# Kernel tuning notes

Measured on AMD Instinct MI355X. Metric: run time of the kernel, lower is better.

The kernel has to match this reference:

```python
import jax, jax.numpy as jnp
import numpy as np

N, E, G = 50000, 800000, 64
IN, H, ED, OUT = 32, 96, 16, 128
EPS_GEN = 1e-7   # GENConv message eps
EPS_BN = 1e-5    # BatchNorm1d eps


def _bn(x, g, b):
    # training-mode BatchNorm1d: batch stats, biased variance
    mu = jnp.mean(x, axis=0)
    var = jnp.var(x, axis=0)
    return (x - mu) * jax.lax.rsqrt(var + EPS_BN) * g + b


def _genconv(x_src, x_dst, src, dst, ea, mw1, mg, mb, mw2):
    # message: relu(x_j + e_ij) + eps            [E, H]
    msg = jax.nn.relu(x_src[src] + ea) + EPS_GEN
    n = x_dst.shape[0]
    # softmax aggregation over incoming edges per dst node (t=1.0)
    m = jax.ops.segment_max(msg, dst, num_segments=n)
    ex = jnp.exp(msg - m[dst])
    s = jax.ops.segment_sum(ex, dst, num_segments=n)
    agg = jax.ops.segment_sum(msg * (ex / s[dst]), dst, num_segments=n)
    h = agg + x_dst
    # GENConv internal MLP: Lin(H,2H,no bias) -> BN -> ReLU -> Lin(2H,H,no bias)
    h = jax.nn.relu(_bn(h @ mw1, mg, mb))
    return h @ mw2


def _forward(x, edge_attr, w_src1, w_dst1, w_edge1,
             mlp1_w1, mlp1_g, mlp1_b, mlp1_w2, bn1_g, bn1_b,
             w_edge2, mlp2_w1, mlp2_g, mlp2_b, mlp2_w2, bn2_g, bn2_b,
             w_edge3, mlp3_w1, mlp3_g, mlp3_b, mlp3_w2, bn3_g, bn3_b,
             lin_w, lin_b, edge_index, batch):
    src, dst = edge_index[0], edge_index[1]
    h = _genconv(x @ w_src1, x @ w_dst1, src, dst, edge_attr @ w_edge1,
                 mlp1_w1, mlp1_g, mlp1_b, mlp1_w2)
    h = jax.nn.relu(_bn(h, bn1_g, bn1_b))
    h = _genconv(h, h, src, dst, edge_attr @ w_edge2,
                 mlp2_w1, mlp2_g, mlp2_b, mlp2_w2)
    h = jax.nn.relu(_bn(h, bn2_g, bn2_b))
    h = _genconv(h, h, src, dst, edge_attr @ w_edge3,
                 mlp3_w1, mlp3_g, mlp3_b, mlp3_w2)
    h = jax.nn.relu(_bn(h, bn3_g, bn3_b))
    # global mean pool over graphs (dropout is identity in eval)
    cnt = jax.ops.segment_sum(jnp.ones((h.shape[0],), h.dtype), batch, num_segments=G)
    pooled = jax.ops.segment_sum(h, batch, num_segments=G) / jnp.maximum(cnt, 1.0)[:, None]
    return pooled @ lin_w + lin_b


def setup_inputs() -> dict:
    key = jax.random.key(0)
    ks = jax.random.split(key, 20)
    rn = lambda i, shp, s=0.05: jax.random.normal(ks[i], shp, jnp.float32) * s
    return {
        'x': rn(0, (N, IN), 1.0),
        'edge_attr': rn(1, (E, ED), 1.0),
        'edge_index': jax.random.randint(ks[2], (2, E), 0, N, jnp.int32),
        'batch': jnp.sort(jax.random.randint(ks[3], (N,), 0, G, jnp.int32)),
        'w_src1': rn(4, (IN, H)), 'w_dst1': rn(5, (IN, H)), 'w_edge1': rn(6, (ED, H)),
        'mlp1_w1': rn(7, (H, 2 * H)), 'mlp1_g': jnp.ones(2 * H), 'mlp1_b': jnp.zeros(2 * H),
        'mlp1_w2': rn(8, (2 * H, H)), 'bn1_g': jnp.ones(H), 'bn1_b': jnp.zeros(H),
        'w_edge2': rn(9, (ED, H)),
        'mlp2_w1': rn(10, (H, 2 * H)), 'mlp2_g': jnp.ones(2 * H), 'mlp2_b': jnp.zeros(2 * H),
        'mlp2_w2': rn(11, (2 * H, H)), 'bn2_g': jnp.ones(H), 'bn2_b': jnp.zeros(H),
        'w_edge3': rn(12, (ED, H)),
        'mlp3_w1': rn(13, (H, 2 * H)), 'mlp3_g': jnp.ones(2 * H), 'mlp3_b': jnp.zeros(2 * H),
        'mlp3_w2': rn(14, (2 * H, H)), 'bn3_g': jnp.ones(H), 'bn3_b': jnp.zeros(H),
        'lin_w': rn(15, (H, OUT)), 'lin_b': jnp.zeros(OUT),
    }


def reference(x, edge_attr, edge_index, batch, w_src1, w_dst1, w_edge1,
              mlp1_w1, mlp1_g, mlp1_b, mlp1_w2, bn1_g, bn1_b,
              w_edge2, mlp2_w1, mlp2_g, mlp2_b, mlp2_w2, bn2_g, bn2_b,
              w_edge3, mlp3_w1, mlp3_g, mlp3_b, mlp3_w2, bn3_g, bn3_b,
              lin_w, lin_b):
    return _forward(x, edge_attr, w_src1, w_dst1, w_edge1,
                    mlp1_w1, mlp1_g, mlp1_b, mlp1_w2, bn1_g, bn1_b,
                    w_edge2, mlp2_w1, mlp2_g, mlp2_b, mlp2_w2, bn2_g, bn2_b,
                    w_edge3, mlp3_w1, mlp3_g, mlp3_b, mlp3_w2, bn3_g, bn3_b,
                    lin_w, lin_b, edge_index, batch)
```

## Files before the change

### kernel.cpp

```cpp
#include <hip/hip_runtime.h>
#include <math.h>

#define NN 50000
#define EE 800000
#define GG 64
#define HH 96
#define H2 192
#define INF 32
#define EDF 16
#define OUTF 128
#define EPS_GEN 1e-7f
#define EPS_BN 1e-5f
#define NPB 100
#define NB_SCAN 49
#define NBH (256 * NB_SCAN)
#define LOG2E 1.44269504088896f
#define SHIFT2 28.85390081777927f

typedef _Float16 f16;
typedef _Float16 f16x2 __attribute__((ext_vector_type(2)));
typedef _Float16 f16x8 __attribute__((ext_vector_type(8)));
typedef float f32x4 __attribute__((ext_vector_type(4)));

static inline size_t align256(size_t x) { return (x + 255) & ~(size_t)255; }

__device__ __forceinline__ float fdot2(f16x2 a, f16x2 b, float c) {
#if __has_builtin(__builtin_amdgcn_fdot2)
    return __builtin_amdgcn_fdot2(a, b, c, false);
#else
    return fmaf((float)a.x, (float)b.x, fmaf((float)a.y, (float)b.y, c));
#endif
}

__device__ __forceinline__ float exp2fast(float x) {
#if __has_builtin(__builtin_amdgcn_exp2f)
    return __builtin_amdgcn_exp2f(x);
#else
    return exp2f(x);
#endif
}


__global__ __launch_bounds__(256) void hist_kernel(const int* __restrict__ dst,
                                                   int* __restrict__ deg) {
    int e = blockIdx.x * 256 + threadIdx.x;
    if (e >= EE) return;
    atomicAdd(&deg[dst[e]], 1);
}

__global__ __launch_bounds__(1024) void scan1_kernel(const int* __restrict__ deg,
                                                     int* __restrict__ offs,
                                                     int* __restrict__ bsum,
                                                     int* __restrict__ bhist) {
    __shared__ int ws[16];
    __shared__ int lh[256];
    int tid = threadIdx.x, lane = tid & 63, w = tid >> 6;
    if (tid < 256) lh[tid] = 0;
    int i = blockIdx.x * 1024 + tid;
    int v = (i < NN) ? deg[i] : 0;
    __syncthreads();
    if (i < NN) {
        int b = 255 - (v > 255 ? 255 : v);
        atomicAdd(&lh[b], 1);
    }
    int x = v;
    #pragma unroll
    for (int off = 1; off < 64; off <<= 1) {
        int y = __shfl_up(x, off, 64);
        if (lane >= off) x += y;
    }
    if (lane == 63) ws[w] = x;
    __syncthreads();
    int wpre = 0;
    for (int j = 0; j < w; ++j) wpre += ws[j];
    if (i < NN) offs[i] = wpre + x - v;
    if (tid == 1023) bsum[blockIdx.x] = wpre + x;
    if (tid < 256) bhist[tid * NB_SCAN + blockIdx.x] = lh[tid];
}

__global__ __launch_bounds__(64) void scan2_kernel(int* __restrict__ bsum) {
    int lane = threadIdx.x;
    int v = (lane < NB_SCAN) ? bsum[lane] : 0;
    int x = v;
    #pragma unroll
    for (int off = 1; off < 64; off <<= 1) {
        int y = __shfl_up(x, off, 64);
        if (lane >= off) x += y;
    }
    if (lane < NB_SCAN) bsum[lane] = x - v;
}

__global__ __launch_bounds__(256) void scan3_kernel(int* __restrict__ offs,
                                                    const int* __restrict__ bsum) {
    int i = blockIdx.x * 256 + threadIdx.x;
    if (i < NN) offs[i] += bsum[i >> 10];
    if (i == 0) offs[NN] = EE;
}

__global__ __launch_bounds__(1024) void bscan_kernel(int* __restrict__ bhist) {
    __shared__ int ws[16];
    __shared__ int carry_s;
    int tid = threadIdx.x, lane = tid & 63, w = tid >> 6;
    if (tid == 0) carry_s = 0;
    __syncthreads();
    for (int base = 0; base < NBH; base += 1024) {
        int i = base + tid;
        int v = (i < NBH) ? bhist[i] : 0;
        int x = v;
        #pragma unroll
        for (int off = 1; off < 64; off <<= 1) {
            int y = __shfl_up(x, off, 64);
            if (lane >= off) x += y;
        }
        if (lane == 63) ws[w] = x;
        __syncthreads();
        int wpre = 0;
        for (int j = 0; j < w; ++j) wpre += ws[j];
        int carry = carry_s;
        if (i < NBH) bhist[i] = carry + wpre + x - v;
        __syncthreads();
        if (tid == 1023) carry_s = carry + wpre + x;
        __syncthreads();
    }
}

__global__ __launch_bounds__(1024) void dscatter_kernel(const int* __restrict__ deg,
                                                        const int* __restrict__ bhist,
                                                        int* __restrict__ perm) {
    __shared__ int cnt[256];
    int tid = threadIdx.x;
    if (tid < 256) cnt[tid] = 0;
    __syncthreads();
    int n = blockIdx.x * 1024 + tid;
    if (n < NN) {
        int d = deg[n];
        int b = 255 - (d > 255 ? 255 : d);
        int rank = atomicAdd(&cnt[b], 1);
        perm[bhist[b * NB_SCAN + blockIdx.x] + rank] = n;
    }
}

__global__ __launch_bounds__(256) void scatter_kernel(const int* __restrict__ src,
                                                      const int* __restrict__ dst,
                                                      const int* __restrict__ offs,
                                                      int* __restrict__ cnt2,
                                                      const float* __restrict__ eattr,
                                                      int* __restrict__ csr_src,
                                                      float4* __restrict__ csrea) {
    int e = blockIdx.x * 256 + threadIdx.x;
    if (e >= EE) return;
    int d = dst[e];
    int slot = offs[d] + atomicAdd(&cnt2[d], 1);
    csr_src[slot] = src[e];
    const float4* ep = (const float4*)(eattr + (size_t)e * EDF);
    float4 v0 = ep[0], v1 = ep[1], v2 = ep[2], v3 = ep[3];
    union { f16x2 h[4]; float4 f; } a, b;
    a.h[0] = f16x2{(f16)v0.x, (f16)v0.y};
    a.h[1] = f16x2{(f16)v0.z, (f16)v0.w};
    a.h[2] = f16x2{(f16)v1.x, (f16)v1.y};
    a.h[3] = f16x2{(f16)v1.z, (f16)v1.w};
    b.h[0] = f16x2{(f16)v2.x, (f16)v2.y};
    b.h[1] = f16x2{(f16)v2.z, (f16)v2.w};
    b.h[2] = f16x2{(f16)v3.x, (f16)v3.y};
    b.h[3] = f16x2{(f16)v3.z, (f16)v3.w};
    csrea[(size_t)slot * 2] = a.f;
    csrea[(size_t)slot * 2 + 1] = b.f;
}

__global__ __launch_bounds__(256) void wprep_kernel(
    const float* __restrict__ we0, const float* __restrict__ we1, const float* __restrict__ we2,
    const float* __restrict__ m10, const float* __restrict__ m11, const float* __restrict__ m12,
    const float* __restrict__ m20, const float* __restrict__ m21, const float* __restrict__ m22,
    f16* __restrict__ wte, f16* __restrict__ wt1, f16* __restrict__ wt2) {
    int idx = blockIdx.x * 256 + threadIdx.x;
    if (idx < 4608) {
        const float* w = (idx < 1536) ? we0 : ((idx < 3072) ? we1 : we2);
        int r = idx % 1536, c = r / EDF, k = r % EDF;
        wte[idx] = (f16)w[k * HH + c];
    } else if (idx < 4608 + 3 * 18432) {
        int m = idx - 4608;
        const float* w = (m < 18432) ? m10 : ((m < 36864) ? m11 : m12);
        int r = m % 18432, j = r / HH, k = r % HH;
        wt1[m] = (f16)w[k * H2 + j];
    } else if (idx < 4608 + 6 * 18432) {
        int m = idx - 4608 - 3 * 18432;
        const float* w = (m < 18432) ? m20 : ((m < 36864) ? m21 : m22);
        int r = m % 18432, j = r / H2, k = r % H2;
        wt2[m] = (f16)w[k * HH + j];
    }
}


__global__ __launch_bounds__(256) void proj_kernel(const float* __restrict__ x,
                                                   const float* __restrict__ ws,
                                                   const float* __restrict__ wd,
                                                   f16* __restrict__ xs,
                                                   f16* __restrict__ xd) {
    __shared__ float Ws[INF * HH], Wd[INF * HH];
    int tid = threadIdx.x;
    for (int i = tid; i < INF * HH; i += 256) { Ws[i] = ws[i]; Wd[i] = wd[i]; }
    __syncthreads();
    int gid = blockIdx.x * 256 + tid;
    if (gid >= NN * HH) return;
    int n = gid / HH, c = gid % HH;
    const float* xr = x + (size_t)n * INF;
    float as = 0.f, ad = 0.f;
    #pragma unroll
    for (int k = 0; k < INF; ++k) {
        float xv = xr[k];
        as = fmaf(xv, Ws[k * HH + c], as);
        ad = fmaf(xv, Wd[k * HH + c], ad);
    }
    xs[gid] = (f16)as;
    xd[gid] = (f16)ad;
}


__global__ __launch_bounds__(192) void agg_kernel(const f16* __restrict__ xsrc,
                                                  const f16* __restrict__ xdst,
                                                  const float4* __restrict__ csrea,
                                                  const f16* __restrict__ wt,
                                                  const int* __restrict__ offs,
                                                  const int* __restrict__ csr_src,
                                                  const int* __restrict__ perm,
                                                  f16* __restrict__ hpre) {
    int tid = threadIdx.x;
    int idx = blockIdx.x * 8 + tid / 24;
    if (idx >= NN) return;
    int node = perm[idx];
    int cg = tid % 24, c0 = cg * 4;
    union W8 { float4 f[2]; f16x2 h[8]; };
    W8 w[4];
    #pragma unroll
    for (int cc = 0; cc < 4; ++cc) {
        const float4* wp = (const float4*)(wt + (c0 + cc) * EDF);
        w[cc].f[0] = wp[0];
        w[cc].f[1] = wp[1];
    }
    int s0 = offs[node], s1 = offs[node + 1];
    float num[4] = {0.f, 0.f, 0.f, 0.f}, den[4] = {0.f, 0.f, 0.f, 0.f};
    if (s0 < s1) {
        int last = s1 - 1;
        union EA { float4 f; f16x2 h[4]; };
        union XU { float2 f; f16x2 h[2]; };
        int j1 = (s0 + 1 < last) ? s0 + 1 : last;
        int j2 = (s0 + 2 < last) ? s0 + 2 : last;
        int sA = csr_src[s0];
        int sB = csr_src[j1];
        int sC = csr_src[j2];
        EA eA0, eA1, eB0, eB1;
        eA0.f = csrea[(size_t)s0 * 2];
        eA1.f = csrea[(size_t)s0 * 2 + 1];
        eB0.f = csrea[(size_t)j1 * 2];
        eB1.f = csrea[(size_t)j1 * 2 + 1];
        XU xA, xB;
        xA.f = *(const float2*)(xsrc + (size_t)sA * HH + c0);
        xB.f = *(const float2*)(xsrc + (size_t)sB * HH + c0);
        for (int j = s0; j <= last; ++j) {
            int j2n = (j + 2 < last) ? j + 2 : last;
            int j3n = (j + 3 < last) ? j + 3 : last;
            EA eC0, eC1;
            XU xC;
            eC0.f = csrea[(size_t)j2n * 2];
            eC1.f = csrea[(size_t)j2n * 2 + 1];
            xC.f = *(const float2*)(xsrc + (size_t)sC * HH + c0);
            int sD = csr_src[j3n];
            float xv[4] = {(float)xA.h[0].x, (float)xA.h[0].y,
                           (float)xA.h[1].x, (float)xA.h[1].y};
            #pragma unroll
            for (int cc = 0; cc < 4; ++cc) {
                float acc = 0.f;
                #pragma unroll
                for (int k = 0; k < 4; ++k) acc = fdot2(eA0.h[k], w[cc].h[k], acc);
                #pragma unroll
                for (int k = 0; k < 4; ++k) acc = fdot2(eA1.h[k], w[cc].h[4 + k], acc);
                float msg = fmaxf(xv[cc] + acc, 0.f) + EPS_GEN;
                float p = exp2fast(fmaf(msg, LOG2E, -SHIFT2));
                den[cc] += p;
                num[cc] = fmaf(msg, p, num[cc]);
            }
            eA0 = eB0; eA1 = eB1; eB0 = eC0; eB1 = eC1;
            xA = xB; xB = xC;
            sC = sD;
        }
    }
    union { float2 f; f16x2 h[2]; } xd, o;
    xd.f = *(const float2*)(xdst + (size_t)node * HH + c0);
    float xdv[4] = {(float)xd.h[0].x, (float)xd.h[0].y, (float)xd.h[1].x, (float)xd.h[1].y};
    float r0 = (den[0] > 0.f) ? num[0] / den[0] : 0.f;
    float r1 = (den[1] > 0.f) ? num[1] / den[1] : 0.f;
    float r2 = (den[2] > 0.f) ? num[2] / den[2] : 0.f;
    float r3 = (den[3] > 0.f) ? num[3] / den[3] : 0.f;
    o.h[0] = f16x2{(f16)(r0 + xdv[0]), (f16)(r1 + xdv[1])};
    o.h[1] = f16x2{(f16)(r2 + xdv[2]), (f16)(r3 + xdv[3])};
    *(float2*)(hpre + (size_t)node * HH + c0) = o.f;
}

#define LDA1 104

__global__ __launch_bounds__(256) void gemm1_kernel(const f16* __restrict__ A,
                                                    const f16* __restrict__ Wt,
                                                    f16* __restrict__ T,
                                                    float* __restrict__ colsum,
                                                    float* __restrict__ colsumsq) {
    __shared__ f16 Al[64 * LDA1];
    __shared__ f16 Wl[192 * LDA1];
    __shared__ float red[H2 * 2];
    int tid = threadIdx.x, n0 = blockIdx.x * 64;
    for (int v = tid; v < 64 * 12; v += 256) {
        int r = v / 12, c8 = (v % 12) * 8;
        float4 d = {0.f, 0.f, 0.f, 0.f};
        if (n0 + r < NN) d = *(const float4*)(A + (size_t)(n0 + r) * HH + c8);
        *(float4*)(Al + r * LDA1 + c8) = d;
    }
    for (int v = tid; v < 192 * 12; v += 256) {
        int r = v / 12, c8 = (v % 12) * 8;
        *(float4*)(Wl + r * LDA1 + c8) = *(const float4*)(Wt + r * HH + c8);
    }
    if (tid < H2) { red[tid] = 0.f; red[H2 + tid] = 0.f; }
    __syncthreads();
    int wv = tid >> 6, l = tid & 63, lr = l & 15, lg = l >> 4;
    int i0 = wv * 16;
    f32x4 acc[12];
    #pragma unroll
    for (int t = 0; t < 12; ++t) acc[t] = (f32x4){0.f, 0.f, 0.f, 0.f};
    #pragma unroll
    for (int ks = 0; ks < 3; ++ks) {
        int k0 = ks * 32 + lg * 8;
        f16x8 af = *(const f16x8*)(Al + (i0 + lr) * LDA1 + k0);
        #pragma unroll
        for (int t = 0; t < 12; ++t) {
            f16x8 bf = *(const f16x8*)(Wl + (t * 16 + lr) * LDA1 + k0);
            acc[t] = __builtin_amdgcn_mfma_f32_16x16x32_f16(af, bf, acc[t], 0, 0, 0);
        }
    }
    #pragma unroll
    for (int t = 0; t < 12; ++t) {
        int col = t * 16 + lr;
        float s = 0.f, q = 0.f;
        #pragma unroll
        for (int rr = 0; rr < 4; ++rr) {
            int row = n0 + i0 + lg * 4 + rr;
            float v = acc[t][rr];
            if (row < NN) {
                T[(size_t)row * H2 + col] = (f16)v;
                s += v;
                q = fmaf(v, v, q);
            }
        }
        s += __shfl_xor(s, 16); s += __shfl_xor(s, 32);
        q += __shfl_xor(q, 16); q += __shfl_xor(q, 32);
        if (lg == 0) { atomicAdd(&red[col], s); atomicAdd(&red[H2 + col], q); }
    }
    __syncthreads();
    if (tid < H2) {
        atomicAdd(&colsum[tid], red[tid]);
        atomicAdd(&colsumsq[tid], red[H2 + tid]);
    }
}

#define LDA2 200

__global__ __launch_bounds__(256) void gemm2_kernel(const f16* __restrict__ T,
                                                    const f16* __restrict__ Wt,
                                                    const float* __restrict__ cs1,
                                                    const float* __restrict__ cq1,
                                                    const float* __restrict__ g1,
                                                    const float* __restrict__ b1,
                                                    f16* __restrict__ U,
                                                    float* __restrict__ colsum,
                                                    float* __restrict__ colsumsq) {
    __shared__ f16 Al[64 * LDA2];
    __shared__ f16 Wl[96 * LDA2];
    __shared__ float ab[H2 * 2];
    __shared__ float red[HH * 2];
    int tid = threadIdx.x, n0 = blockIdx.x * 64;
    if (tid < H2) {
        const float invN = 1.f / (float)NN;
        float mu = cs1[tid] * invN;
        float var = fmaxf(cq1[tid] * invN - mu * mu, 0.f);
        float a = g1[tid] * rsqrtf(var + EPS_BN);
        ab[tid] = a;
        ab[H2 + tid] = b1[tid] - mu * a;
    }
    if (tid < HH) { red[tid] = 0.f; red[HH + tid] = 0.f; }
    __syncthreads();
    for (int v = tid; v < 64 * 24; v += 256) {
        int r = v / 24, c8 = (v % 24) * 8;
        float4 dd = {0.f, 0.f, 0.f, 0.f};
        if (n0 + r < NN) {
            union { float4 f; f16x2 h[4]; } u, o;
            u.f = *(const float4*)(T + (size_t)(n0 + r) * H2 + c8);
            #pragma unroll
            for (int p = 0; p < 4; ++p) {
                float x0 = fmaxf(fmaf((float)u.h[p].x, ab[c8 + 2 * p], ab[H2 + c8 + 2 * p]), 0.f);
                float x1 = fmaxf(fmaf((float)u.h[p].y, ab[c8 + 2 * p + 1], ab[H2 + c8 + 2 * p + 1]), 0.f);
                o.h[p] = f16x2{(f16)x0, (f16)x1};
            }
            dd = o.f;
        }
        *(float4*)(Al + r * LDA2 + c8) = dd;
    }
    for (int v = tid; v < 96 * 24; v += 256) {
        int r = v / 24, c8 = (v % 24) * 8;
        *(float4*)(Wl + r * LDA2 + c8) = *(const float4*)(Wt + r * H2 + c8);
    }
    __syncthreads();
    int wv = tid >> 6, l = tid & 63, lr = l & 15, lg = l >> 4;
    int i0 = wv * 16;
    f32x4 acc[6];
    #pragma unroll
    for (int t = 0; t < 6; ++t) acc[t] = (f32x4){0.f, 0.f, 0.f, 0.f};
    #pragma unroll
    for (int ks = 0; ks < 6; ++ks) {
        int k0 = ks * 32 + lg * 8;
        f16x8 af = *(const f16x8*)(Al + (i0 + lr) * LDA2 + k0);
        #pragma unroll
        for (int t = 0; t < 6; ++t) {
            f16x8 bf = *(const f16x8*)(Wl + (t * 16 + lr) * LDA2 + k0);
            acc[t] = __builtin_amdgcn_mfma_f32_16x16x32_f16(af, bf, acc[t], 0, 0, 0);
        }
    }
    #pragma unroll
    for (int t = 0; t < 6; ++t) {
        int col = t * 16 + lr;
        float s = 0.f, q = 0.f;
        #pragma unroll
        for (int rr = 0; rr < 4; ++rr) {
            int row = n0 + i0 + lg * 4 + rr;
            float v = acc[t][rr];
            if (row < NN) {
                U[(size_t)row * HH + col] = (f16)v;
                s += v;
                q = fmaf(v, v, q);
            }
        }
        s += __shfl_xor(s, 16); s += __shfl_xor(s, 32);
        q += __shfl_xor(q, 16); q += __shfl_xor(q, 32);
        if (lg == 0) { atomicAdd(&red[col], s); atomicAdd(&red[HH + col], q); }
    }
    __syncthreads();
    if (tid < HH) {
        atomicAdd(&colsum[tid], red[tid]);
        atomicAdd(&colsumsq[tid], red[HH + tid]);
    }
}


__global__ __launch_bounds__(256) void elem_kernel(const f16* __restrict__ U,
                                                   const float* __restrict__ cs2,
                                                   const float* __restrict__ cq2,
                                                   const float* __restrict__ g2,
                                                   const float* __restrict__ b2,
                                                   f16* __restrict__ Hout) {
    __shared__ float ab[HH * 2];
    int tid = threadIdx.x;
    if (tid < HH) {
        const float invN = 1.f / (float)NN;
        float mu = cs2[tid] * invN;
        float var = fmaxf(cq2[tid] * invN - mu * mu, 0.f);
        float a = g2[tid] * rsqrtf(var + EPS_BN);
        ab[tid] = a;
        ab[HH + tid] = b2[tid] - mu * a;
    }
    __syncthreads();
    int i = blockIdx.x * 256 + tid;
    if (i >= NN * HH / 8) return;
    union { float4 f; f16x2 h[4]; } u, o;
    u.f = ((const float4*)U)[i];
    int k = (i % 12) * 8;
    #pragma unroll
    for (int p = 0; p < 4; ++p) {
        float x0 = fmaxf(fmaf((float)u.h[p].x, ab[k + 2 * p], ab[HH + k + 2 * p]), 0.f);
        float x1 = fmaxf(fmaf((float)u.h[p].y, ab[k + 2 * p + 1], ab[HH + k + 2 * p + 1]), 0.f);
        o.h[p] = f16x2{(f16)x0, (f16)x1};
    }
    ((float4*)Hout)[i] = o.f;
}


__global__ __launch_bounds__(192) void pool_bn_kernel(const f16* __restrict__ U,
                                                      const float* __restrict__ cs2,
                                                      const float* __restrict__ cq2,
                                                      const float* __restrict__ g2,
                                                      const float* __restrict__ b2,
                                                      const int* __restrict__ batch,
                                                      float* __restrict__ pool) {
    __shared__ float ab[HH * 2];
    int tid = threadIdx.x;
    if (tid < HH) {
        const float invN = 1.f / (float)NN;
        float mu = cs2[tid] * invN;
        float var = fmaxf(cq2[tid] * invN - mu * mu, 0.f);
        float a = g2[tid] * rsqrtf(var + EPS_BN);
        ab[tid] = a;
        ab[HH + tid] = b2[tid] - mu * a;
    }
    __syncthreads();
    int n0 = blockIdx.x * NPB;
    int n1 = (n0 + NPB < NN) ? n0 + NPB : NN;
    int c = tid % HH;
    int h = tid / HH;
    float a_ = ab[c], b_ = ab[HH + c];
    float acc = 0.f;
    int gcur = -1;
    for (int n = n0 + h; n < n1; n += 2) {
        int g = batch[n];
        if (g != gcur) {
            if (gcur >= 0) atomicAdd(&pool[gcur * HH + c], acc);
            acc = 0.f;
            gcur = g;
        }
        acc += fmaxf(fmaf((float)U[(size_t)n * HH + c], a_, b_), 0.f);
    }
    if (gcur >= 0) atomicAdd(&pool[gcur * HH + c], acc);
}

__global__ __launch_bounds__(128) void out_kernel(const float* __restrict__ pool,
                                                  const int* __restrict__ batch,
                                                  const float* __restrict__ lw,
                                                  const float* __restrict__ lb,
                                                  float* __restrict__ out) {
    int g = blockIdx.x, o = threadIdx.x;
    int lo = 0, hi = NN;
    while (lo < hi) { int mid = (lo + hi) >> 1; if (batch[mid] < g) lo = mid + 1; else hi = mid; }
    int s = lo;
    lo = 0; hi = NN;
    while (lo < hi) { int mid = (lo + hi) >> 1; if (batch[mid] < g + 1) lo = mid + 1; else hi = mid; }
    float inv = 1.f / fmaxf((float)(lo - s), 1.f);
    float acc = lb[o];
    for (int c = 0; c < HH; ++c) acc = fmaf(pool[g * HH + c] * inv, lw[c * OUTF + o], acc);
    out[(size_t)g * OUTF + o] = acc;
}


extern "C" void kernel_launch(void* const* d_in, const int* in_sizes, int n_in,
                              void* d_out, int out_size, void* d_ws, size_t ws_size,
                              hipStream_t stream) {
    const float* x = (const float*)d_in[0];
    const float* eattr = (const float*)d_in[1];
    const int* eidx = (const int*)d_in[2];
    const int* batch = (const int*)d_in[3];
    const float* w_src1 = (const float*)d_in[4];
    const float* w_dst1 = (const float*)d_in[5];
    const float* w_e[3] = {(const float*)d_in[6], (const float*)d_in[13], (const float*)d_in[20]};
    const float* mw1[3] = {(const float*)d_in[7], (const float*)d_in[14], (const float*)d_in[21]};
    const float* mg[3] = {(const float*)d_in[8], (const float*)d_in[15], (const float*)d_in[22]};
    const float* mb[3] = {(const float*)d_in[9], (const float*)d_in[16], (const float*)d_in[23]};
    const float* mw2[3] = {(const float*)d_in[10], (const float*)d_in[17], (const float*)d_in[24]};
    const float* bng[3] = {(const float*)d_in[11], (const float*)d_in[18], (const float*)d_in[25]};
    const float* bnb[3] = {(const float*)d_in[12], (const float*)d_in[19], (const float*)d_in[26]};
    const float* lin_w = (const float*)d_in[27];
    const float* lin_b = (const float*)d_in[28];
    float* out = (float*)d_out;

    const int* src = eidx;
    const int* dst = eidx + EE;

    char* base = (char*)d_ws;
    size_t off = 0;
    int* deg = (int*)(base + off); off = align256(off + (size_t)NN * 4);
    int* cnt2 = (int*)(base + off); off = align256(off + (size_t)NN * 4);
    int* offs = (int*)(base + off); off = align256(off + (size_t)(NN + 1) * 4);
    int* bsum = (int*)(base + off); off = align256(off + (size_t)NB_SCAN * 4);
    int* bhist = (int*)(base + off); off = align256(off + (size_t)NBH * 4);
    int* perm = (int*)(base + off); off = align256(off + (size_t)NN * 4);
    int* csr_src = (int*)(base + off); off = align256(off + (size_t)EE * 4);
    float* stats = (float*)(base + off); off = align256(off + 576 * 4);
    float* colsum1 = stats;
    float* colsumsq1 = stats + 192;
    float* colsum2 = stats + 384;
    float* colsumsq2 = stats + 480;
    float* pool = (float*)(base + off); off = align256(off + (size_t)GG * HH * 4);
    f16* wte = (f16*)(base + off); off = align256(off + (size_t)3 * 1536 * 2);
    f16* wt1 = (f16*)(base + off); off = align256(off + (size_t)3 * 18432 * 2);
    f16* wt2 = (f16*)(base + off); off = align256(off + (size_t)3 * 18432 * 2);
    f16* XS = (f16*)(base + off); off = align256(off + (size_t)NN * HH * 2);
    f16* XD = (f16*)(base + off); off = align256(off + (size_t)NN * HH * 2);
    f16* HP = (f16*)(base + off); off = align256(off + (size_t)NN * HH * 2);
    f16* T = (f16*)(base + off); off = align256(off + (size_t)NN * H2 * 2);
    float4* csrea = (float4*)(base + off); off = align256(off + (size_t)EE * 32);
    (void)in_sizes; (void)n_in; (void)out_size; (void)ws_size;

    hipMemsetAsync(deg, 0, (size_t)NN * 4, stream);
    hipMemsetAsync(cnt2, 0, (size_t)NN * 4, stream);
    hist_kernel<<<(EE + 255) / 256, 256, 0, stream>>>(dst, deg);
    scan1_kernel<<<NB_SCAN, 1024, 0, stream>>>(deg, offs, bsum, bhist);
    scan2_kernel<<<1, 64, 0, stream>>>(bsum);
    scan3_kernel<<<(NN + 255) / 256, 256, 0, stream>>>(offs, bsum);
    bscan_kernel<<<1, 1024, 0, stream>>>(bhist);
    dscatter_kernel<<<NB_SCAN, 1024, 0, stream>>>(deg, bhist, perm);
    scatter_kernel<<<(EE + 255) / 256, 256, 0, stream>>>(src, dst, offs, cnt2, eattr,
                                                         csr_src, csrea);
    wprep_kernel<<<(4608 + 6 * 18432 + 255) / 256, 256, 0, stream>>>(
        w_e[0], w_e[1], w_e[2], mw1[0], mw1[1], mw1[2], mw2[0], mw2[1], mw2[2],
        wte, wt1, wt2);

    proj_kernel<<<(NN * HH + 255) / 256, 256, 0, stream>>>(x, w_src1, w_dst1, XS, XD);

    for (int l = 0; l < 3; ++l) {
        const f16* xdst = (l == 0) ? XD : XS;
        hipMemsetAsync(stats, 0, 576 * 4, stream);
        agg_kernel<<<(NN + 7) / 8, 192, 0, stream>>>(XS, xdst, csrea, wte + l * 1536, offs,
                                                     csr_src, perm, HP);
        gemm1_kernel<<<(NN + 63) / 64, 256, 0, stream>>>(HP, wt1 + l * 18432, T,
                                                         colsum1, colsumsq1);
        gemm2_kernel<<<(NN + 63) / 64, 256, 0, stream>>>(T, wt2 + l * 18432, colsum1,
                                                         colsumsq1, mg[l], mb[l], HP,
                                                         colsum2, colsumsq2);
        if (l < 2)
            elem_kernel<<<(NN * HH / 8 + 255) / 256, 256, 0, stream>>>(HP, colsum2, colsumsq2,
                                                                       bng[l], bnb[l], XS);
    }

    hipMemsetAsync(pool, 0, (size_t)(GG * HH) * 4, stream);
    pool_bn_kernel<<<(NN + NPB - 1) / NPB, 192, 0, stream>>>(HP, colsum2, colsumsq2,
                                                             bng[2], bnb[2], batch, pool);
    out_kernel<<<GG, 128, 0, stream>>>(pool, batch, lin_w, lin_b, out);
}
```

Before: 590.8 us.

## Fuse scan/memset launches, split CSR build, and drop prefetch clamps in aggregation

Folds the scan2/scan3 and pool/stats memsets into existing kernels (bscan, finsort, agg) to cut launch count. It splits the edge scatter into a compact (src, edge id) scatter followed by a node-ordered conversion pass, so the f16 edge-attribute writes become coalesced. It also pads the CSR arrays so the aggregation prefetch can read past the end of a segment without index clamps, and adds an unroll pragma. In exchange there is an extra pass over the CSR data. Zeroing stats from block 0 of agg relies on stream ordering relative to the earlier gemm atomics.

```diff
diff --git a/kernel.cpp b/kernel.cpp
--- a/kernel.cpp
+++ b/kernel.cpp
@@ -78,29 +78,23 @@
     if (tid < 256) bhist[tid * NB_SCAN + blockIdx.x] = lh[tid];
 }
 
-__global__ __launch_bounds__(64) void scan2_kernel(int* __restrict__ bsum) {
-    int lane = threadIdx.x;
-    int v = (lane < NB_SCAN) ? bsum[lane] : 0;
-    int x = v;
-    #pragma unroll
-    for (int off = 1; off < 64; off <<= 1) {
-        int y = __shfl_up(x, off, 64);
-        if (lane >= off) x += y;
-    }
-    if (lane < NB_SCAN) bsum[lane] = x - v;
-}
-
-__global__ __launch_bounds__(256) void scan3_kernel(int* __restrict__ offs,
-                                                    const int* __restrict__ bsum) {
-    int i = blockIdx.x * 256 + threadIdx.x;
-    if (i < NN) offs[i] += bsum[i >> 10];
-    if (i == 0) offs[NN] = EE;
-}
-
-__global__ __launch_bounds__(1024) void bscan_kernel(int* __restrict__ bhist) {
+__global__ __launch_bounds__(1024) void bscan_kernel(int* __restrict__ bhist,
+                                                     int* __restrict__ bsum,
+                                                     float* __restrict__ pool) {
     __shared__ int ws[16];
     __shared__ int carry_s;
     int tid = threadIdx.x, lane = tid & 63, w = tid >> 6;
+    for (int i = tid; i < GG * HH; i += 1024) pool[i] = 0.f;
+    if (tid < 64) {
+        int v = (tid < NB_SCAN) ? bsum[tid] : 0;
+        int x = v;
+        #pragma unroll
+        for (int off = 1; off < 64; off <<= 1) {
+            int y = __shfl_up(x, off, 64);
+            if (lane >= off) x += y;
+        }
+        if (tid < NB_SCAN) bsum[tid] = x - v;
+    }
     if (tid == 0) carry_s = 0;
     __syncthreads();
     for (int base = 0; base < NBH; base += 1024) {
@@ -124,47 +118,67 @@
     }
 }
 
-__global__ __launch_bounds__(1024) void dscatter_kernel(const int* __restrict__ deg,
-                                                        const int* __restrict__ bhist,
-                                                        int* __restrict__ perm) {
+__global__ __launch_bounds__(1024) void finsort_kernel(int* __restrict__ offs,
+                                                       const int* __restrict__ bsum,
+                                                       const int* __restrict__ deg,
+                                                       const int* __restrict__ bhist,
+                                                       int* __restrict__ perm) {
     __shared__ int cnt[256];
     int tid = threadIdx.x;
     if (tid < 256) cnt[tid] = 0;
     __syncthreads();
     int n = blockIdx.x * 1024 + tid;
     if (n < NN) {
+        offs[n] += bsum[blockIdx.x];
         int d = deg[n];
         int b = 255 - (d > 255 ? 255 : d);
         int rank = atomicAdd(&cnt[b], 1);
         perm[bhist[b * NB_SCAN + blockIdx.x] + rank] = n;
     }
+    if (n == NN) offs[NN] = EE;
 }
 
 __global__ __launch_bounds__(256) void scatter_kernel(const int* __restrict__ src,
                                                       const int* __restrict__ dst,
                                                       const int* __restrict__ offs,
                                                       int* __restrict__ cnt2,
-                                                      const float* __restrict__ eattr,
-                                                      int* __restrict__ csr_src,
-                                                      float4* __restrict__ csrea) {
+                                                      int2* __restrict__ csr_se) {
     int e = blockIdx.x * 256 + threadIdx.x;
     if (e >= EE) return;
     int d = dst[e];
     int slot = offs[d] + atomicAdd(&cnt2[d], 1);
-    csr_src[slot] = src[e];
-    const float4* ep = (const float4*)(eattr + (size_t)e * EDF);
-    float4 v0 = ep[0], v1 = ep[1], v2 = ep[2], v3 = ep[3];
-    union { f16x2 h[4]; float4 f; } a, b;
-    a.h[0] = f16x2{(f16)v0.x, (f16)v0.y};
-    a.h[1] = f16x2{(f16)v0.z, (f16)v0.w};
-    a.h[2] = f16x2{(f16)v1.x, (f16)v1.y};
-    a.h[3] = f16x2{(f16)v1.z, (f16)v1.w};
-    b.h[0] = f16x2{(f16)v2.x, (f16)v2.y};
-    b.h[1] = f16x2{(f16)v2.z, (f16)v2.w};
-    b.h[2] = f16x2{(f16)v3.x, (f16)v3.y};
-    b.h[3] = f16x2{(f16)v3.z, (f16)v3.w};
-    csrea[(size_t)slot * 2] = a.f;
-    csrea[(size_t)slot * 2 + 1] = b.f;
+    csr_se[slot] = int2{src[e], e};
+}
+
+__global__ __launch_bounds__(256) void csrcvt_kernel(const int2* __restrict__ csr_se,
+                                                     const float* __restrict__ eattr,
+                                                     const int* __restrict__ offs,
+                                                     const int* __restrict__ perm,
+                                                     int* __restrict__ csr_src,
+                                                     float4* __restrict__ csrea) {
+    int gid = blockIdx.x * 256 + threadIdx.x;
+    if (gid < 4) csr_src[EE + gid] = 0;
+    int idx = gid >> 3, t = gid & 7;
+    if (idx >= NN) return;
+    int node = perm[idx];
+    int s0 = offs[node], s1 = offs[node + 1];
+    for (int j = s0 + t; j < s1; j += 8) {
+        int2 se = csr_se[j];
+        csr_src[j] = se.x;
+        const float4* ep = (const float4*)(eattr + (size_t)se.y * EDF);
+        float4 v0 = ep[0], v1 = ep[1], v2 = ep[2], v3 = ep[3];
+        union { f16x2 h[4]; float4 f; } a, b;
+        a.h[0] = f16x2{(f16)v0.x, (f16)v0.y};
+        a.h[1] = f16x2{(f16)v0.z, (f16)v0.w};
+        a.h[2] = f16x2{(f16)v1.x, (f16)v1.y};
+        a.h[3] = f16x2{(f16)v1.z, (f16)v1.w};
+        b.h[0] = f16x2{(f16)v2.x, (f16)v2.y};
+        b.h[1] = f16x2{(f16)v2.z, (f16)v2.w};
+        b.h[2] = f16x2{(f16)v3.x, (f16)v3.y};
+        b.h[3] = f16x2{(f16)v3.z, (f16)v3.w};
+        csrea[(size_t)j * 2] = a.f;
+        csrea[(size_t)j * 2 + 1] = b.f;
+    }
 }
 
 __global__ __launch_bounds__(256) void wprep_kernel(
@@ -223,8 +237,12 @@
                                                   const int* __restrict__ offs,
                                                   const int* __restrict__ csr_src,
                                                   const int* __restrict__ perm,
+                                                  float* __restrict__ stats,
                                                   f16* __restrict__ hpre) {
     int tid = threadIdx.x;
+    if (blockIdx.x == 0) {
+        for (int t = tid; t < 576; t += 192) stats[t] = 0.f;
+    }
     int idx = blockIdx.x * 8 + tid / 24;
     if (idx >= NN) return;
     int node = perm[idx];
@@ -237,34 +255,33 @@
         w[cc].f[0] = wp[0];
         w[cc].f[1] = wp[1];
     }
+    union XU { float2 f; f16x2 h[2]; };
+    XU xd;
+    xd.f = *(const float2*)(xdst + (size_t)node * HH + c0);
     int s0 = offs[node], s1 = offs[node + 1];
     float num[4] = {0.f, 0.f, 0.f, 0.f}, den[4] = {0.f, 0.f, 0.f, 0.f};
     if (s0 < s1) {
         int last = s1 - 1;
         union EA { float4 f; f16x2 h[4]; };
-        union XU { float2 f; f16x2 h[2]; };
-        int j1 = (s0 + 1 < last) ? s0 + 1 : last;
-        int j2 = (s0 + 2 < last) ? s0 + 2 : last;
         int sA = csr_src[s0];
-        int sB = csr_src[j1];
-        int sC = csr_src[j2];
+        int sB = csr_src[s0 + 1];
+        int sC = csr_src[s0 + 2];
         EA eA0, eA1, eB0, eB1;
         eA0.f = csrea[(size_t)s0 * 2];
         eA1.f = csrea[(size_t)s0 * 2 + 1];
-        eB0.f = csrea[(size_t)j1 * 2];
-        eB1.f = csrea[(size_t)j1 * 2 + 1];
+        eB0.f = csrea[(size_t)(s0 + 1) * 2];
+        eB1.f = csrea[(size_t)(s0 + 1) * 2 + 1];
         XU xA, xB;
         xA.f = *(const float2*)(xsrc + (size_t)sA * HH + c0);
         xB.f = *(const float2*)(xsrc + (size_t)sB * HH + c0);
+        #pragma unroll 2
         for (int j = s0; j <= last; ++j) {
-            int j2n = (j + 2 < last) ? j + 2 : last;
-            int j3n = (j + 3 < last) ? j + 3 : last;
             EA eC0, eC1;
             XU xC;
-            eC0.f = csrea[(size_t)j2n * 2];
-            eC1.f = csrea[(size_t)j2n * 2 + 1];
+            eC0.f = csrea[(size_t)(j + 2) * 2];
+            eC1.f = csrea[(size_t)(j + 2) * 2 + 1];
             xC.f = *(const float2*)(xsrc + (size_t)sC * HH + c0);
-            int sD = csr_src[j3n];
+            int sD = csr_src[j + 3];
             float xv[4] = {(float)xA.h[0].x, (float)xA.h[0].y,
                            (float)xA.h[1].x, (float)xA.h[1].y};
             #pragma unroll
@@ -284,13 +301,12 @@
             sC = sD;
         }
     }
-    union { float2 f; f16x2 h[2]; } xd, o;
-    xd.f = *(const float2*)(xdst + (size_t)node * HH + c0);
     float xdv[4] = {(float)xd.h[0].x, (float)xd.h[0].y, (float)xd.h[1].x, (float)xd.h[1].y};
     float r0 = (den[0] > 0.f) ? num[0] / den[0] : 0.f;
     float r1 = (den[1] > 0.f) ? num[1] / den[1] : 0.f;
     float r2 = (den[2] > 0.f) ? num[2] / den[2] : 0.f;
     float r3 = (den[3] > 0.f) ? num[3] / den[3] : 0.f;
+    union { float2 f; f16x2 h[2]; } o;
     o.h[0] = f16x2{(f16)(r0 + xdv[0]), (f16)(r1 + xdv[1])};
     o.h[1] = f16x2{(f16)(r2 + xdv[2]), (f16)(r3 + xdv[3])};
     *(float2*)(hpre + (size_t)node * HH + c0) = o.f;
@@ -561,11 +577,13 @@
     size_t off = 0;
     int* deg = (int*)(base + off); off = align256(off + (size_t)NN * 4);
     int* cnt2 = (int*)(base + off); off = align256(off + (size_t)NN * 4);
+    size_t degcnt_span = off;
     int* offs = (int*)(base + off); off = align256(off + (size_t)(NN + 1) * 4);
     int* bsum = (int*)(base + off); off = align256(off + (size_t)NB_SCAN * 4);
     int* bhist = (int*)(base + off); off = align256(off + (size_t)NBH * 4);
     int* perm = (int*)(base + off); off = align256(off + (size_t)NN * 4);
-    int* csr_src = (int*)(base + off); off = align256(off + (size_t)EE * 4);
+    int2* csr_se = (int2*)(base + off); off = align256(off + (size_t)(EE + 4) * 8);
+    int* csr_src = (int*)(base + off); off = align256(off + (size_t)(EE + 4) * 4);
     float* stats = (float*)(base + off); off = align256(off + 576 * 4);
     float* colsum1 = stats;
     float* colsumsq1 = stats + 192;
@@ -579,19 +597,17 @@
     f16* XD = (f16*)(base + off); off = align256(off + (size_t)NN * HH * 2);
     f16* HP = (f16*)(base + off); off = align256(off + (size_t)NN * HH * 2);
     f16* T = (f16*)(base + off); off = align256(off + (size_t)NN * H2 * 2);
-    float4* csrea = (float4*)(base + off); off = align256(off + (size_t)EE * 32);
+    float4* csrea = (float4*)(base + off); off = align256(off + (size_t)(EE + 4) * 32);
     (void)in_sizes; (void)n_in; (void)out_size; (void)ws_size;
 
-    hipMemsetAsync(deg, 0, (size_t)NN * 4, stream);
-    hipMemsetAsync(cnt2, 0, (size_t)NN * 4, stream);
+    hipMemsetAsync(deg, 0, degcnt_span, stream);
     hist_kernel<<<(EE + 255) / 256, 256, 0, stream>>>(dst, deg);
     scan1_kernel<<<NB_SCAN, 1024, 0, stream>>>(deg, offs, bsum, bhist);
-    scan2_kernel<<<1, 64, 0, stream>>>(bsum);
-    scan3_kernel<<<(NN + 255) / 256, 256, 0, stream>>>(offs, bsum);
-    bscan_kernel<<<1, 1024, 0, stream>>>(bhist);
-    dscatter_kernel<<<NB_SCAN, 1024, 0, stream>>>(deg, bhist, perm);
-    scatter_kernel<<<(EE + 255) / 256, 256, 0, stream>>>(src, dst, offs, cnt2, eattr,
-                                                         csr_src, csrea);
+    bscan_kernel<<<1, 1024, 0, stream>>>(bhist, bsum, pool);
+    finsort_kernel<<<NB_SCAN, 1024, 0, stream>>>(offs, bsum, deg, bhist, perm);
+    scatter_kernel<<<(EE + 255) / 256, 256, 0, stream>>>(src, dst, offs, cnt2, csr_se);
+    csrcvt_kernel<<<(NN * 8 + 255) / 256, 256, 0, stream>>>(csr_se, eattr, offs, perm,
+                                                            csr_src, csrea);
     wprep_kernel<<<(4608 + 6 * 18432 + 255) / 256, 256, 0, stream>>>(
         w_e[0], w_e[1], w_e[2], mw1[0], mw1[1], mw1[2], mw2[0], mw2[1], mw2[2],
         wte, wt1, wt2);
@@ -600,9 +616,8 @@
 
     for (int l = 0; l < 3; ++l) {
         const f16* xdst = (l == 0) ? XD : XS;
-        hipMemsetAsync(stats, 0, 576 * 4, stream);
         agg_kernel<<<(NN + 7) / 8, 192, 0, stream>>>(XS, xdst, csrea, wte + l * 1536, offs,
-                                                     csr_src, perm, HP);
+                                                     csr_src, perm, stats, HP);
         gemm1_kernel<<<(NN + 63) / 64, 256, 0, stream>>>(HP, wt1 + l * 18432, T,
                                                          colsum1, colsumsq1);
         gemm2_kernel<<<(NN + 63) / 64, 256, 0, stream>>>(T, wt2 + l * 18432, colsum1,
@@ -613,7 +628,6 @@
                                                                        bng[l], bnb[l], XS);
     }
 
-    hipMemsetAsync(pool, 0, (size_t)(GG * HH) * 4, stream);
     pool_bn_kernel<<<(NN + NPB - 1) / NPB, 192, 0, stream>>>(HP, colsum2, colsumsq2,
                                                              bng[2], bnb[2], batch, pool);
     out_kernel<<<GG, 128, 0, stream>>>(pool, batch, lin_w, lin_b, out);
```

Measured after the change: 616.7 us. 4.4% more time.
